# Performance work log

Measured on AMD Instinct MI355X. Metric: run time of the kernel, lower is better.

## Reference

```python
import jax, jax.numpy as jnp
import numpy as np

TAU_MIN = 0.001
XPBD_ITERS = 4
XPBD_COMPLIANCE = 0.0
XPBD_MAX_CORR = 0.15

B, N, D, E = 4, 50000, 256, 800000


def setup_inputs() -> dict:
    key = jax.random.key(0)
    ks = jax.random.split(key, 7)
    keypoints = jax.random.normal(ks[0], (B, N, 3), dtype=jnp.float32)
    timesteps = jax.random.uniform(ks[1], (B,), dtype=jnp.float32)
    hand_tokens = jax.random.normal(ks[2], (B, N, D), dtype=jnp.float32)
    head_w = jax.random.normal(ks[3], (D, 3), dtype=jnp.float32) * 0.02
    head_b = jnp.zeros((3,), dtype=jnp.float32)
    edge_index = jax.random.randint(ks[4], (2, E), 0, N, dtype=jnp.int32)
    rest_lengths = jax.random.uniform(ks[5], (E,), dtype=jnp.float32) + 0.1
    return {
        "keypoints": keypoints,
        "timesteps": timesteps,
        "hand_tokens": hand_tokens,
        "head_w": head_w,
        "head_b": head_b,
        "edge_index": edge_index,
        "rest_lengths": rest_lengths,
    }


def _xpbd_project(x, src, dst, rest_lengths):
    # x: (B, N, 3); src/dst: (E,); rest_lengths: (E,)
    L0 = rest_lengths[None, :, None]          # (1, E, 1)
    w_i = 1.0                                  # inv_mass is None -> unit inverse masses
    w_j = 1.0
    alpha = XPBD_COMPLIANCE / (float(XPBD_ITERS) + 1e-08)
    denom = w_i + w_j + alpha + 1e-09
    for _ in range(XPBD_ITERS):
        diff = x[:, src] - x[:, dst]           # (B, E, 3) edge gather
        dist = jnp.linalg.norm(diff, axis=-1, keepdims=True)  # (B, E, 1)
        C = dist - L0
        n = diff / (dist + 1e-09)
        d_lambda = -C / denom
        correction = jnp.clip(d_lambda * n, -XPBD_MAX_CORR, XPBD_MAX_CORR)
        delta = (jnp.zeros_like(x)
                 .at[:, src].add(w_i * correction)
                 .at[:, dst].add(-w_j * correction))  # scatter-add back to nodes
        x = x + delta
    return x


def reference(keypoints, timesteps, hand_tokens, head_w, head_b, edge_index, rest_lengths):
    # tau = clamp(1 - t, min=tau_min), broadcast to (B, 1, 1)
    tau = jnp.maximum(1.0 - timesteps, TAU_MIN)[:, None, None]
    v_raw = hand_tokens @ head_w + head_b      # (B, N, 3) velocity head
    x_pred = keypoints + tau * v_raw
    src = edge_index[0]
    dst = edge_index[1]
    x_corrected = _xpbd_project(x_pred, src, dst, rest_lengths)
    v_eff = (x_corrected - keypoints) / tau
    return v_eff
```

## Files before the change

### kernel.cpp

```cpp
#include <hip/hip_runtime.h>

#define BB 4
#define NN 50000
#define DD 256
#define EE 800000
#define TAU_MIN_F 0.001f
#define MAX_CORR_F 0.15f

#define CAP 80
#define NPART 8
#define PNODES (NN / NPART)
#define PS_CE 2048
#define PS_NCHUNK ((EE + PS_CE - 1) / PS_CE)
#define NBUCKET (NPART * PS_NCHUNK)
#define XPB 2048
#define NWAVE (XPB * 4)

typedef float  f4 __attribute__((ext_vector_type(4)));
typedef int    i2 __attribute__((ext_vector_type(2)));

__device__ __forceinline__ float wsum64(float x) {
    x += __int_as_float(__builtin_amdgcn_update_dpp(0, __float_as_int(x), 0x111, 0xf, 0xf, true));
    x += __int_as_float(__builtin_amdgcn_update_dpp(0, __float_as_int(x), 0x112, 0xf, 0xf, true));
    x += __int_as_float(__builtin_amdgcn_update_dpp(0, __float_as_int(x), 0x114, 0xf, 0xf, true));
    x += __int_as_float(__builtin_amdgcn_update_dpp(0, __float_as_int(x), 0x118, 0xf, 0xf, true));
    x += __int_as_float(__builtin_amdgcn_update_dpp(0, __float_as_int(x), 0x142, 0xf, 0xf, true));
    x += __int_as_float(__builtin_amdgcn_update_dpp(0, __float_as_int(x), 0x143, 0xf, 0xf, true));
    return x;
}

__global__ __launch_bounds__(256) void xpred_kernel(
    const float* __restrict__ kp, const float* __restrict__ ts,
    const float* __restrict__ ht, const float* __restrict__ hw,
    const float* __restrict__ hb, float4* __restrict__ x)
{
    const int lane = threadIdx.x & 63;
    const int wave = ((int)blockIdx.x * 256 + (int)threadIdx.x) >> 6;
    const int d0   = lane * 4;

    float W[4][3];
#pragma unroll
    for (int j = 0; j < 4; ++j)
#pragma unroll
        for (int k = 0; k < 3; ++k)
            W[j][k] = hw[(d0 + j) * 3 + k];
    const float b0 = hb[0], b1 = hb[1], b2 = hb[2];

    int i = wave;
    for (; i + NWAVE < BB * NN; i += 2 * NWAVE) {
        const int iA = i, iB = i + NWAVE;
        const int rowA = (iA & 3) * NN + (iA >> 2);
        const int rowB = (iB & 3) * NN + (iB >> 2);
        const f4 hA = __builtin_nontemporal_load((const f4*)(ht + (size_t)rowA * DD + d0));
        const f4 hB = __builtin_nontemporal_load((const f4*)(ht + (size_t)rowB * DD + d0));
        float aA0 = hA.x * W[0][0] + hA.y * W[1][0] + hA.z * W[2][0] + hA.w * W[3][0];
        float aA1 = hA.x * W[0][1] + hA.y * W[1][1] + hA.z * W[2][1] + hA.w * W[3][1];
        float aA2 = hA.x * W[0][2] + hA.y * W[1][2] + hA.z * W[2][2] + hA.w * W[3][2];
        float aB0 = hB.x * W[0][0] + hB.y * W[1][0] + hB.z * W[2][0] + hB.w * W[3][0];
        float aB1 = hB.x * W[0][1] + hB.y * W[1][1] + hB.z * W[2][1] + hB.w * W[3][1];
        float aB2 = hB.x * W[0][2] + hB.y * W[1][2] + hB.z * W[2][2] + hB.w * W[3][2];
        aA0 = wsum64(aA0);  aB0 = wsum64(aB0);
        aA1 = wsum64(aA1);  aB1 = wsum64(aB1);
        aA2 = wsum64(aA2);  aB2 = wsum64(aB2);
        if (lane == 63) {
            {
                const float tau = fmaxf(1.0f - ts[iA & 3], TAU_MIN_F);
                float4 v;
                v.x = kp[rowA * 3 + 0] + tau * (aA0 + b0);
                v.y = kp[rowA * 3 + 1] + tau * (aA1 + b1);
                v.z = kp[rowA * 3 + 2] + tau * (aA2 + b2);
                v.w = 0.0f;
                x[iA] = v;
            }
            {
                const float tau = fmaxf(1.0f - ts[iB & 3], TAU_MIN_F);
                float4 v;
                v.x = kp[rowB * 3 + 0] + tau * (aB0 + b0);
                v.y = kp[rowB * 3 + 1] + tau * (aB1 + b1);
                v.z = kp[rowB * 3 + 2] + tau * (aB2 + b2);
                v.w = 0.0f;
                x[iB] = v;
            }
        }
    }
    if (i < BB * NN) {
        const int row = (i & 3) * NN + (i >> 2);
        const f4 h = __builtin_nontemporal_load((const f4*)(ht + (size_t)row * DD + d0));
        float a0 = h.x * W[0][0] + h.y * W[1][0] + h.z * W[2][0] + h.w * W[3][0];
        float a1 = h.x * W[0][1] + h.y * W[1][1] + h.z * W[2][1] + h.w * W[3][1];
        float a2 = h.x * W[0][2] + h.y * W[1][2] + h.z * W[2][2] + h.w * W[3][2];
        a0 = wsum64(a0);  a1 = wsum64(a1);  a2 = wsum64(a2);
        if (lane == 63) {
            const float tau = fmaxf(1.0f - ts[i & 3], TAU_MIN_F);
            float4 v;
            v.x = kp[row * 3 + 0] + tau * (a0 + b0);
            v.y = kp[row * 3 + 1] + tau * (a1 + b1);
            v.z = kp[row * 3 + 2] + tau * (a2 + b2);
            v.w = 0.0f;
            x[i] = v;
        }
    }
}

__global__ __launch_bounds__(256) void pbucket_kernel(
    const int* __restrict__ ei, const float* __restrict__ L0,
    int* __restrict__ counts, int2* __restrict__ adj)
{
    const int part  = (int)blockIdx.x & 7;
    const int chunk = (int)blockIdx.x >> 3;
    const int lo   = part * PNODES;
    const int hi   = lo + PNODES;
    const int base = chunk * PS_CE;
    const int eEnd = min(base + PS_CE, EE);
    for (int e = base + (int)threadIdx.x; e < eEnd; e += 256) {
        const int s = __builtin_nontemporal_load(ei + e);
        const int d = __builtin_nontemporal_load(ei + EE + e);
        const int r = __float_as_int(__builtin_nontemporal_load(L0 + e));
        const bool hs = (s >= lo) & (s < hi);
        const bool hd = (d >= lo) & (d < hi);
        int ps = CAP, pd = CAP;
        if (hs) ps = atomicAdd(&counts[s], 1);
        if (hd) pd = atomicAdd(&counts[d], 1);
        if (hs && ps < CAP) adj[s * CAP + ps] = make_int2(d << 2, r);
        if (hd && pd < CAP) adj[d * CAP + pd] = make_int2(s << 2, r);
    }
}

__global__ __launch_bounds__(256) void gather_kernel(
    const float4* __restrict__ xin, float4* __restrict__ xout,
    const int* __restrict__ counts, const int2* __restrict__ adj,
    const float* __restrict__ kp, const float* __restrict__ ts,
    float* __restrict__ out, int final_iter)
{
    const int tid  = blockIdx.x * 256 + threadIdx.x;
    const int b    = tid & 3;
    const int sub  = (tid >> 2) & 7;
    const int node = tid >> 5;

    const float4 xc = xin[(node << 2) + b];
    float a0 = 0.0f, a1 = 0.0f, a2 = 0.0f;

    const int beg = node * CAP;
    const int cnt = min(counts[node], CAP);
    const int seg = ((cnt + 15) >> 4) << 1;
    int k        = beg + sub * seg;
    const int ke = min(k + seg, beg + cnt);

    for (; k + 1 < ke; k += 2) {
        const int4 e = *(const int4*)(&adj[k]);
        const float4 n0 = xin[e.x + b];
        const float4 n1 = xin[e.z + b];
        {
            const float dx = xc.x - n0.x, dy = xc.y - n0.y, dz = xc.z - n0.z;
            const float dist = sqrtf(dx * dx + dy * dy + dz * dz);
            const float s = (__int_as_float(e.y) - dist) * 0.5f / (dist + 1e-9f);
            a0 += fminf(fmaxf(s * dx, -MAX_CORR_F), MAX_CORR_F);
            a1 += fminf(fmaxf(s * dy, -MAX_CORR_F), MAX_CORR_F);
            a2 += fminf(fmaxf(s * dz, -MAX_CORR_F), MAX_CORR_F);
        }
        {
            const float dx = xc.x - n1.x, dy = xc.y - n1.y, dz = xc.z - n1.z;
            const float dist = sqrtf(dx * dx + dy * dy + dz * dz);
            const float s = (__int_as_float(e.w) - dist) * 0.5f / (dist + 1e-9f);
            a0 += fminf(fmaxf(s * dx, -MAX_CORR_F), MAX_CORR_F);
            a1 += fminf(fmaxf(s * dy, -MAX_CORR_F), MAX_CORR_F);
            a2 += fminf(fmaxf(s * dz, -MAX_CORR_F), MAX_CORR_F);
        }
    }
    if (k < ke) {
        const int2 e0 = adj[k];
        const float4 n0 = xin[e0.x + b];
        const float dx = xc.x - n0.x, dy = xc.y - n0.y, dz = xc.z - n0.z;
        const float dist = sqrtf(dx * dx + dy * dy + dz * dz);
        const float s = (__int_as_float(e0.y) - dist) * 0.5f / (dist + 1e-9f);
        a0 += fminf(fmaxf(s * dx, -MAX_CORR_F), MAX_CORR_F);
        a1 += fminf(fmaxf(s * dy, -MAX_CORR_F), MAX_CORR_F);
        a2 += fminf(fmaxf(s * dz, -MAX_CORR_F), MAX_CORR_F);
    }

    a0 += __shfl_xor(a0, 4);  a0 += __shfl_xor(a0, 8);  a0 += __shfl_xor(a0, 16);
    a1 += __shfl_xor(a1, 4);  a1 += __shfl_xor(a1, 8);  a1 += __shfl_xor(a1, 16);
    a2 += __shfl_xor(a2, 4);  a2 += __shfl_xor(a2, 8);  a2 += __shfl_xor(a2, 16);

    if (sub == 0) {
        if (!final_iter) {
            float4 v; v.x = xc.x + a0; v.y = xc.y + a1; v.z = xc.z + a2; v.w = 0.0f;
            xout[(node << 2) + b] = v;
        } else {
            const int row = b * NN + node;
            const float tau = fmaxf(1.0f - ts[b], TAU_MIN_F);
            const float itau = 1.0f / tau;
            __builtin_nontemporal_store((xc.x + a0 - kp[row * 3 + 0]) * itau, out + row * 3 + 0);
            __builtin_nontemporal_store((xc.y + a1 - kp[row * 3 + 1]) * itau, out + row * 3 + 1);
            __builtin_nontemporal_store((xc.z + a2 - kp[row * 3 + 2]) * itau, out + row * 3 + 2);
        }
    }
}

extern "C" void kernel_launch(void* const* d_in, const int* in_sizes, int n_in,
                              void* d_out, int out_size, void* d_ws, size_t ws_size,
                              hipStream_t stream)
{
    const float* kp = (const float*)d_in[0];
    const float* ts = (const float*)d_in[1];
    const float* ht = (const float*)d_in[2];
    const float* hw = (const float*)d_in[3];
    const float* hb = (const float*)d_in[4];
    const int*   ei = (const int*)d_in[5];
    const float* L0 = (const float*)d_in[6];
    float* out = (float*)d_out;

    char* w = (char*)d_ws;
    int2*   adj    = (int2*)w;                 w += (size_t)NN * CAP * sizeof(int2);
    float4* xA     = (float4*)w;               w += (size_t)BB * NN * sizeof(float4);
    float4* xB     = (float4*)w;               w += (size_t)BB * NN * sizeof(float4);
    int*    counts = (int*)w;

    hipMemsetAsync(counts, 0, (size_t)NN * sizeof(int), stream);

    xpred_kernel<<<XPB, 256, 0, stream>>>(kp, ts, ht, hw, hb, xA);
    pbucket_kernel<<<NBUCKET, 256, 0, stream>>>(ei, L0, counts, adj);

    const int gatherBlocks = (32 * NN) / 256;
    gather_kernel<<<gatherBlocks, 256, 0, stream>>>(xA, xB, counts, adj, kp, ts, out, 0);
    gather_kernel<<<gatherBlocks, 256, 0, stream>>>(xB, xA, counts, adj, kp, ts, out, 0);
    gather_kernel<<<gatherBlocks, 256, 0, stream>>>(xA, xB, counts, adj, kp, ts, out, 0);
    gather_kernel<<<gatherBlocks, 256, 0, stream>>>(xB, xA, counts, adj, kp, ts, out, 1);
}
```

Baseline: 448.5 us.

## Fuse four XPBD gather iterations into one persistent kernel with grid barrier

Replaces the four separate gather launches with a single persistent kernel of 1792 blocks that loops over all node slots and runs all four iterations. Between iterations it uses an atomic-counter grid barrier with a sleep-wait loop, and the barrier counter is zeroed along with the counts array. This removes three kernel launch gaps and the tail effects between them. In exchange, every block must be resident at once (launch_bounds 7 blocks per CU), and the barrier spin adds its own overhead and a risk of deadlock if the grid does not fit. The barrier has a guard timeout that could break correctness if it triggers.

Measured after the change: 1.378 ms. +207.3%, slower.

```diff
diff --git a/kernel.cpp b/kernel.cpp
--- a/kernel.cpp
+++ b/kernel.cpp
@@ -15,6 +15,9 @@
 #define NBUCKET (NPART * PS_NCHUNK)
 #define XPB 2048
 #define NWAVE (XPB * 4)
+
+#define GB 1792
+#define GT (GB * 256)
 
 typedef float  f4 __attribute__((ext_vector_type(4)));
 typedef int    i2 __attribute__((ext_vector_type(2)));
@@ -126,73 +129,98 @@
     }
 }
 
-__global__ __launch_bounds__(256) void gather_kernel(
-    const float4* __restrict__ xin, float4* __restrict__ xout,
+__global__ __launch_bounds__(256, 7) void solve_kernel(
+    float4* __restrict__ xA, float4* __restrict__ xB,
     const int* __restrict__ counts, const int2* __restrict__ adj,
     const float* __restrict__ kp, const float* __restrict__ ts,
-    float* __restrict__ out, int final_iter)
-{
-    const int tid  = blockIdx.x * 256 + threadIdx.x;
-    const int b    = tid & 3;
-    const int sub  = (tid >> 2) & 7;
-    const int node = tid >> 5;
-
-    const float4 xc = xin[(node << 2) + b];
-    float a0 = 0.0f, a1 = 0.0f, a2 = 0.0f;
-
-    const int beg = node * CAP;
-    const int cnt = min(counts[node], CAP);
-    const int seg = ((cnt + 15) >> 4) << 1;
-    int k        = beg + sub * seg;
-    const int ke = min(k + seg, beg + cnt);
-
-    for (; k + 1 < ke; k += 2) {
-        const int4 e = *(const int4*)(&adj[k]);
-        const float4 n0 = xin[e.x + b];
-        const float4 n1 = xin[e.z + b];
-        {
-            const float dx = xc.x - n0.x, dy = xc.y - n0.y, dz = xc.z - n0.z;
-            const float dist = sqrtf(dx * dx + dy * dy + dz * dz);
-            const float s = (__int_as_float(e.y) - dist) * 0.5f / (dist + 1e-9f);
-            a0 += fminf(fmaxf(s * dx, -MAX_CORR_F), MAX_CORR_F);
-            a1 += fminf(fmaxf(s * dy, -MAX_CORR_F), MAX_CORR_F);
-            a2 += fminf(fmaxf(s * dz, -MAX_CORR_F), MAX_CORR_F);
-        }
-        {
-            const float dx = xc.x - n1.x, dy = xc.y - n1.y, dz = xc.z - n1.z;
-            const float dist = sqrtf(dx * dx + dy * dy + dz * dz);
-            const float s = (__int_as_float(e.w) - dist) * 0.5f / (dist + 1e-9f);
-            a0 += fminf(fmaxf(s * dx, -MAX_CORR_F), MAX_CORR_F);
-            a1 += fminf(fmaxf(s * dy, -MAX_CORR_F), MAX_CORR_F);
-            a2 += fminf(fmaxf(s * dz, -MAX_CORR_F), MAX_CORR_F);
-        }
-    }
-    if (k < ke) {
-        const int2 e0 = adj[k];
-        const float4 n0 = xin[e0.x + b];
-        const float dx = xc.x - n0.x, dy = xc.y - n0.y, dz = xc.z - n0.z;
-        const float dist = sqrtf(dx * dx + dy * dy + dz * dz);
-        const float s = (__int_as_float(e0.y) - dist) * 0.5f / (dist + 1e-9f);
-        a0 += fminf(fmaxf(s * dx, -MAX_CORR_F), MAX_CORR_F);
-        a1 += fminf(fmaxf(s * dy, -MAX_CORR_F), MAX_CORR_F);
-        a2 += fminf(fmaxf(s * dz, -MAX_CORR_F), MAX_CORR_F);
-    }
-
-    a0 += __shfl_xor(a0, 4);  a0 += __shfl_xor(a0, 8);  a0 += __shfl_xor(a0, 16);
-    a1 += __shfl_xor(a1, 4);  a1 += __shfl_xor(a1, 8);  a1 += __shfl_xor(a1, 16);
-    a2 += __shfl_xor(a2, 4);  a2 += __shfl_xor(a2, 8);  a2 += __shfl_xor(a2, 16);
-
-    if (sub == 0) {
-        if (!final_iter) {
-            float4 v; v.x = xc.x + a0; v.y = xc.y + a1; v.z = xc.z + a2; v.w = 0.0f;
-            xout[(node << 2) + b] = v;
-        } else {
-            const int row = b * NN + node;
-            const float tau = fmaxf(1.0f - ts[b], TAU_MIN_F);
-            const float itau = 1.0f / tau;
-            __builtin_nontemporal_store((xc.x + a0 - kp[row * 3 + 0]) * itau, out + row * 3 + 0);
-            __builtin_nontemporal_store((xc.y + a1 - kp[row * 3 + 1]) * itau, out + row * 3 + 1);
-            __builtin_nontemporal_store((xc.z + a2 - kp[row * 3 + 2]) * itau, out + row * 3 + 2);
+    float* __restrict__ out, int* __restrict__ bar)
+{
+    const int gtid = (int)blockIdx.x * 256 + (int)threadIdx.x;
+
+    for (int it = 0; it < 4; ++it) {
+        const float4* __restrict__ xin  = (it & 1) ? xB : xA;
+        float4*       __restrict__ xout = (it & 1) ? xA : xB;
+        const bool final_iter = (it == 3);
+
+        for (int slot = gtid; slot < 32 * NN; slot += GT) {
+            const int b    = slot & 3;
+            const int sub  = (slot >> 2) & 7;
+            const int node = slot >> 5;
+
+            const float4 xc = xin[(node << 2) + b];
+            float a0 = 0.0f, a1 = 0.0f, a2 = 0.0f;
+
+            const int beg = node * CAP;
+            const int cnt = min(counts[node], CAP);
+            const int seg = ((cnt + 15) >> 4) << 1;
+            int k        = beg + sub * seg;
+            const int ke = min(k + seg, beg + cnt);
+
+            for (; k + 1 < ke; k += 2) {
+                const int4 e = *(const int4*)(&adj[k]);
+                const float4 n0 = xin[e.x + b];
+                const float4 n1 = xin[e.z + b];
+                {
+                    const float dx = xc.x - n0.x, dy = xc.y - n0.y, dz = xc.z - n0.z;
+                    const float dist = sqrtf(dx * dx + dy * dy + dz * dz);
+                    const float s = (__int_as_float(e.y) - dist) * 0.5f / (dist + 1e-9f);
+                    a0 += fminf(fmaxf(s * dx, -MAX_CORR_F), MAX_CORR_F);
+                    a1 += fminf(fmaxf(s * dy, -MAX_CORR_F), MAX_CORR_F);
+                    a2 += fminf(fmaxf(s * dz, -MAX_CORR_F), MAX_CORR_F);
+                }
+                {
+                    const float dx = xc.x - n1.x, dy = xc.y - n1.y, dz = xc.z - n1.z;
+                    const float dist = sqrtf(dx * dx + dy * dy + dz * dz);
+                    const float s = (__int_as_float(e.w) - dist) * 0.5f / (dist + 1e-9f);
+                    a0 += fminf(fmaxf(s * dx, -MAX_CORR_F), MAX_CORR_F);
+                    a1 += fminf(fmaxf(s * dy, -MAX_CORR_F), MAX_CORR_F);
+                    a2 += fminf(fmaxf(s * dz, -MAX_CORR_F), MAX_CORR_F);
+                }
+            }
+            if (k < ke) {
+                const int2 e0 = adj[k];
+                const float4 n0 = xin[e0.x + b];
+                const float dx = xc.x - n0.x, dy = xc.y - n0.y, dz = xc.z - n0.z;
+                const float dist = sqrtf(dx * dx + dy * dy + dz * dz);
+                const float s = (__int_as_float(e0.y) - dist) * 0.5f / (dist + 1e-9f);
+                a0 += fminf(fmaxf(s * dx, -MAX_CORR_F), MAX_CORR_F);
+                a1 += fminf(fmaxf(s * dy, -MAX_CORR_F), MAX_CORR_F);
+                a2 += fminf(fmaxf(s * dz, -MAX_CORR_F), MAX_CORR_F);
+            }
+
+            a0 += __shfl_xor(a0, 4);  a0 += __shfl_xor(a0, 8);  a0 += __shfl_xor(a0, 16);
+            a1 += __shfl_xor(a1, 4);  a1 += __shfl_xor(a1, 8);  a1 += __shfl_xor(a1, 16);
+            a2 += __shfl_xor(a2, 4);  a2 += __shfl_xor(a2, 8);  a2 += __shfl_xor(a2, 16);
+
+            if (sub == 0) {
+                if (!final_iter) {
+                    float4 v; v.x = xc.x + a0; v.y = xc.y + a1; v.z = xc.z + a2; v.w = 0.0f;
+                    xout[(node << 2) + b] = v;
+                } else {
+                    const int row = b * NN + node;
+                    const float tau = fmaxf(1.0f - ts[b], TAU_MIN_F);
+                    const float itau = 1.0f / tau;
+                    __builtin_nontemporal_store((xc.x + a0 - kp[row * 3 + 0]) * itau, out + row * 3 + 0);
+                    __builtin_nontemporal_store((xc.y + a1 - kp[row * 3 + 1]) * itau, out + row * 3 + 1);
+                    __builtin_nontemporal_store((xc.z + a2 - kp[row * 3 + 2]) * itau, out + row * 3 + 2);
+                }
+            }
+        }
+
+        if (it < 3) {
+            __threadfence();
+            __syncthreads();
+            if (threadIdx.x == 0) {
+                __hip_atomic_fetch_add(bar, 1, __ATOMIC_RELEASE, __HIP_MEMORY_SCOPE_AGENT);
+                const int target = GB * (it + 1);
+                int guard = 0;
+                while (__hip_atomic_load(bar, __ATOMIC_RELAXED, __HIP_MEMORY_SCOPE_AGENT) < target) {
+                    __builtin_amdgcn_s_sleep(4);
+                    if (++guard > (1 << 22)) break;
+                }
+                __builtin_amdgcn_fence(__ATOMIC_ACQUIRE, "agent");
+            }
+            __syncthreads();
         }
     }
 }
@@ -215,15 +243,12 @@
     float4* xA     = (float4*)w;               w += (size_t)BB * NN * sizeof(float4);
     float4* xB     = (float4*)w;               w += (size_t)BB * NN * sizeof(float4);
     int*    counts = (int*)w;
-
-    hipMemsetAsync(counts, 0, (size_t)NN * sizeof(int), stream);
+    int*    bar    = counts + NN;
+
+    hipMemsetAsync(counts, 0, (size_t)(NN + 1) * sizeof(int), stream);
 
     xpred_kernel<<<XPB, 256, 0, stream>>>(kp, ts, ht, hw, hb, xA);
     pbucket_kernel<<<NBUCKET, 256, 0, stream>>>(ei, L0, counts, adj);
 
-    const int gatherBlocks = (32 * NN) / 256;
-    gather_kernel<<<gatherBlocks, 256, 0, stream>>>(xA, xB, counts, adj, kp, ts, out, 0);
-    gather_kernel<<<gatherBlocks, 256, 0, stream>>>(xB, xA, counts, adj, kp, ts, out, 0);
-    gather_kernel<<<gatherBlocks, 256, 0, stream>>>(xA, xB, counts, adj, kp, ts, out, 0);
-    gather_kernel<<<gatherBlocks, 256, 0, stream>>>(xB, xA, counts, adj, kp, ts, out, 1);
-}
+    solve_kernel<<<GB, 256, 0, stream>>>(xA, xB, counts, adj, kp, ts, out, bar);
+}
```
